# Kernel tuning notes

Hardware: AMD Instinct MI355X
Metric: run time of the kernel (lower is better)

The kernel has to match this reference:

```python
import jax, jax.numpy as jnp
import numpy as np

B, T, D, H = 4, 2048, 1024, 16
DK = DV = 64
R = 64
KS = 4
EPS = 1e-6


def setup_inputs() -> dict:
    key = jax.random.key(0)
    ks = jax.random.split(key, 16)
    def w(k, shape, s=0.02):
        return jax.random.normal(k, shape, jnp.float32) * s
    return {
        "x": jax.random.normal(ks[0], (B, T, D), jnp.float32),
        "conv_q_w": w(ks[1], (D, 1, KS), 0.3), "conv_q_b": jnp.zeros((D,), jnp.float32),
        "conv_k_w": w(ks[2], (D, 1, KS), 0.3), "conv_k_b": jnp.zeros((D,), jnp.float32),
        "conv_v_w": w(ks[3], (D, 1, KS), 0.3), "conv_v_b": jnp.zeros((D,), jnp.float32),
        "Wq": w(ks[4], (D, H * DK)), "bq": jnp.zeros((H * DK,), jnp.float32),
        "Wk": w(ks[5], (D, H * DK)), "bk": jnp.zeros((H * DK,), jnp.float32),
        "Wv": w(ks[6], (D, H * DV)), "bv": jnp.zeros((H * DV,), jnp.float32),
        "W_ad": w(ks[7], (D, R)), "b_ad": jnp.zeros((R,), jnp.float32),
        "W_au": w(ks[8], (R, H * DK)), "b_au": jnp.zeros((H * DK,), jnp.float32),
        "W_beta": w(ks[9], (D, H)), "b_beta": jnp.zeros((H,), jnp.float32),
        "rms_w": jnp.ones((H, DV), jnp.float32),
        "W_gd": w(ks[10], (D, R)), "b_gd": jnp.zeros((R,), jnp.float32),
        "W_gu": w(ks[11], (R, H)), "b_gu": jnp.zeros((H,), jnp.float32),
        "Wo": w(ks[12], (H * DV, D)), "bo": jnp.zeros((D,), jnp.float32),
    }


def _shortconv(x, w, b):
    # causal depthwise conv1d: torch pads (KS-1) both sides then slices [:T] == left-pad KS-1
    xc = jnp.transpose(x, (0, 2, 1))  # [B, D, T]
    y = jax.lax.conv_general_dilated(
        xc, w, (1,), [(KS - 1, 0)],
        dimension_numbers=("NCH", "OIH", "NCH"), feature_group_count=D)
    y = y + b[None, :, None]
    return jax.nn.silu(jnp.transpose(y, (0, 2, 1)))  # [B, T, D]


def _l2(x):
    # x / sqrt(clamp(sum(x^2), eps))  (matches torch clamp_min then sqrt)
    return x / jnp.sqrt(jnp.maximum(jnp.sum(x * x, -1, keepdims=True), EPS))


def _heads(z, dh):
    # [B,T,H*dh] -> [B*H,T,dh]
    return jnp.transpose(z.reshape(B, T, H, dh), (0, 2, 1, 3)).reshape(B * H, T, dh)


def reference(x, conv_q_w, conv_q_b, conv_k_w, conv_k_b, conv_v_w, conv_v_b,
              Wq, bq, Wk, bk, Wv, bv, W_ad, b_ad, W_au, b_au, W_beta, b_beta,
              rms_w, W_gd, b_gd, W_gu, b_gu, Wo, bo):
    qx = _shortconv(x, conv_q_w, conv_q_b)
    kx = _shortconv(x, conv_k_w, conv_k_b)
    vx = _shortconv(x, conv_v_w, conv_v_b)
    Q = _l2(_heads(qx @ Wq + bq, DK))            # [BH,T,DK]
    K = _l2(_heads(kx @ Wk + bk, DK))            # [BH,T,DK]
    V = _heads(vx @ Wv + bv, DV)                 # [BH,T,DV]
    alpha = jax.nn.sigmoid(jax.nn.silu(x @ W_ad + b_ad) @ W_au + b_au)  # [B,T,H*DK]
    A = _heads(alpha, DK)                        # [BH,T,DK]
    beta = jax.nn.sigmoid(x @ W_beta + b_beta)   # [B,T,H]
    Bta = jnp.transpose(beta, (0, 2, 1)).reshape(B * H, T, 1)

    S0 = jnp.zeros((B * H, DK, DV), jnp.float32)

    def step(S, inp):
        q, k, v, a, b = inp                      # [BH,DK],[BH,DK],[BH,DV],[BH,DK],[BH,1]
        S = S * a[:, :, None]                    # gated decay (row scale)
        kTS = jnp.einsum("bi,bij->bj", k, S)    # k^T S : [BH,DV]
        S = S + (b * k)[:, :, None] * (v - kTS)[:, None, :]  # rank-1 delta update
        o = jnp.einsum("bij,bi->bj", S, q)      # S^T q : [BH,DV]
        return S, o

    tm = lambda z: jnp.transpose(z, (1, 0, 2))   # time-major for scan
    S_final, out_t = jax.lax.scan(step, S0, (tm(Q), tm(K), tm(V), tm(A), tm(Bta)))
    O = jnp.transpose(out_t, (1, 0, 2)).reshape(B, H, T, DV)

    # headwise RMSNorm then sigmoid output gate
    var = jnp.mean(O * O, -1, keepdims=True)
    O = O * jax.lax.rsqrt(var + EPS) * rms_w[None, :, None, :]
    gate = jax.nn.sigmoid(jax.nn.silu(x @ W_gd + b_gd) @ W_gu + b_gu)  # [B,T,H]
    O = O * jnp.transpose(gate, (0, 2, 1))[:, :, :, None]

    y = jnp.transpose(O, (0, 2, 1, 3)).reshape(B, T, H * DV) @ Wo + bo
    return y, S_final.reshape(B, H, DK, DV)
```

## Files before the change

### kernel.cpp

```cpp
#include <hip/hip_runtime.h>
#include <hip/hip_bf16.h>
#include <cstdint>

#define BB 4
#define TT 2048
#define DD 1024
#define HH 16
#define NR (BB*TT)
#define CC 16
#define NCH (TT/CC)

typedef __attribute__((ext_vector_type(8))) short bf16x8;
typedef __attribute__((ext_vector_type(4))) float f32x4;
typedef __attribute__((ext_vector_type(4))) unsigned int u32x4;
typedef __attribute__((ext_vector_type(2))) unsigned int u32x2;

#define GLL(g, l, SZ) __builtin_amdgcn_global_load_lds( \
    (const __attribute__((address_space(1))) void*)(uintptr_t)(const void*)(g), \
    (__attribute__((address_space(3))) void*)(uintptr_t)(void*)(l), SZ, 0, 0)

__device__ __forceinline__ unsigned short f2bf(float f) {
  unsigned u = __builtin_bit_cast(unsigned, f);
  unsigned r = 0x7FFFu + ((u >> 16) & 1u);
  return (unsigned short)((u + r) >> 16);
}
__device__ __forceinline__ unsigned pk2(float a, float b) {
  return (unsigned)f2bf(a) | ((unsigned)f2bf(b) << 16);
}
__device__ __forceinline__ float siluf(float v) { return v / (1.f + __expf(-v)); }
__device__ __forceinline__ float sigmf(float v) { return 1.f / (1.f + __expf(-v)); }


__global__ __launch_bounds__(256) void transpose_convert(
    const float* __restrict__ W, unsigned short* __restrict__ Wt, int K, int N) {
  __shared__ float tile[64][65];
  const int tid = threadIdx.x;
  const int bk = blockIdx.x * 64, bn = blockIdx.y * 64;
  const int r = tid >> 2, c4 = (tid & 3) * 16;
#pragma unroll 4
  for (int e = 0; e < 16; ++e)
    tile[r][c4 + e] = W[(size_t)(bk + r) * N + bn + c4 + e];
  __syncthreads();
#pragma unroll 4
  for (int e = 0; e < 16; ++e)
    Wt[(size_t)(bn + r) * K + bk + c4 + e] = f2bf(tile[c4 + e][r]);
}

__global__ void conv_small_T(const float* __restrict__ W, unsigned short* __restrict__ Wt,
                             int K, int N, int Npad) {
  int idx = blockIdx.x * 256 + threadIdx.x;
  if (idx >= Npad * K) return;
  int n = idx / K, k = idx - n * K;
  float v = (n < N) ? W[(size_t)k * N + n] : 0.f;
  Wt[idx] = f2bf(v);
}

__global__ void pack_stage1_T(const float* __restrict__ Wad, const float* __restrict__ Wgd,
                              const float* __restrict__ Wbeta, unsigned short* __restrict__ Wt) {
  int idx = blockIdx.x * 256 + threadIdx.x;
  int n = idx >> 10, k = idx & 1023;
  float v = 0.f;
  if (n < 64) v = Wad[(size_t)k * 64 + n];
  else if (n < 128) v = Wgd[(size_t)k * 64 + (n - 64)];
  else if (n < 144) v = Wbeta[(size_t)k * 16 + (n - 128)];
  Wt[idx] = f2bf(v);
}

__global__ void pack_bias(const float* __restrict__ bad, const float* __restrict__ bgd,
                          const float* __restrict__ bbeta, const float* __restrict__ bgu,
                          float* __restrict__ bst1, float* __restrict__ bgup) {
  int t = threadIdx.x;
  float v = 0.f;
  if (t < 64) v = bad[t];
  else if (t < 128) v = bgd[t - 64];
  else if (t < 144) v = bbeta[t - 128];
  bst1[t] = v;
  if (t < 128) bgup[t] = (t < 16) ? bgu[t] : 0.f;
}

__global__ __launch_bounds__(256) void conv_silu(
    const float* __restrict__ x,
    const float* __restrict__ qw, const float* __restrict__ qb,
    const float* __restrict__ kw, const float* __restrict__ kb,
    const float* __restrict__ vw, const float* __restrict__ vb,
    unsigned short* __restrict__ qx, unsigned short* __restrict__ kx,
    unsigned short* __restrict__ vx, unsigned short* __restrict__ xb) {
  const int n = blockIdx.x;
  const int t = n & (TT - 1);
  const int d0 = threadIdx.x * 4;
  const size_t base = (size_t)n * DD + d0;
  f32x4 zero = {0.f, 0.f, 0.f, 0.f};
  f32x4 x0 = *(const f32x4*)(x + base);
  f32x4 xm1 = (t >= 1) ? *(const f32x4*)(x + base - DD) : zero;
  f32x4 xm2 = (t >= 2) ? *(const f32x4*)(x + base - 2 * DD) : zero;
  f32x4 xm3 = (t >= 3) ? *(const f32x4*)(x + base - 3 * DD) : zero;
  float sq[4], sk[4], sv[4];
#pragma unroll
  for (int e = 0; e < 4; ++e) {
    const int d = d0 + e;
    const f32x4 wq = *(const f32x4*)(qw + (size_t)d * 4);
    const f32x4 wk = *(const f32x4*)(kw + (size_t)d * 4);
    const f32x4 wv = *(const f32x4*)(vw + (size_t)d * 4);
    float aq = wq[0] * xm3[e] + wq[1] * xm2[e] + wq[2] * xm1[e] + wq[3] * x0[e] + qb[d];
    float ak = wk[0] * xm3[e] + wk[1] * xm2[e] + wk[2] * xm1[e] + wk[3] * x0[e] + kb[d];
    float av = wv[0] * xm3[e] + wv[1] * xm2[e] + wv[2] * xm1[e] + wv[3] * x0[e] + vb[d];
    sq[e] = siluf(aq); sk[e] = siluf(ak); sv[e] = siluf(av);
  }
  u32x2 o;
  o[0] = pk2(sq[0], sq[1]); o[1] = pk2(sq[2], sq[3]); *(u32x2*)(qx + base) = o;
  o[0] = pk2(sk[0], sk[1]); o[1] = pk2(sk[2], sk[3]); *(u32x2*)(kx + base) = o;
  o[0] = pk2(sv[0], sv[1]); o[1] = pk2(sv[2], sv[3]); *(u32x2*)(vx + base) = o;
  o[0] = pk2(x0[0], x0[1]); o[1] = pk2(x0[2], x0[3]); *(u32x2*)(xb + base) = o;
}

template <int ACT>
__global__ __launch_bounds__(256) void gemm_bt(
    const unsigned short* __restrict__ A, const unsigned short* __restrict__ Bt,
    const float* __restrict__ bias, float* __restrict__ C,
    int M, int N, int K, int ldc, int nstore) {
  __shared__ unsigned short lsA[128 * 32];
  __shared__ unsigned short lsB[128 * 32];
  const int tid = threadIdx.x;
  const int wid = tid >> 6, lane = tid & 63;
  const int wr = wid >> 1, wc = wid & 1;
  const int m0 = blockIdx.x * 128, n0 = blockIdx.y * 128;
  f32x4 acc[4][4] = {};
  const int nk = K >> 5;
  const int r0 = wid * 32 + (lane >> 2);
  const int cb = (lane & 3) * 16;
  char* lA = (char*)lsA;
  char* lB = (char*)lsB;
  const size_t rowb = (size_t)K * 2;

  for (int kt = 0; kt < nk; ++kt) {
    const char* gA = (const char*)(A + (size_t)(m0 + r0) * K) + kt * 64 + cb;
    const char* gB = (const char*)(Bt + (size_t)(n0 + r0) * K) + kt * 64 + cb;
    GLL(gA, lA + (wid * 32) * 64, 16);
    GLL(gA + 16 * rowb, lA + (wid * 32 + 16) * 64, 16);
    GLL(gB, lB + (wid * 32) * 64, 16);
    GLL(gB + 16 * rowb, lB + (wid * 32 + 16) * 64, 16);
    __syncthreads();
    bf16x8 af[4], bfr[4];
#pragma unroll
    for (int f = 0; f < 4; ++f)
      af[f] = *(const bf16x8*)(lA + (wr * 64 + f * 16 + (lane & 15)) * 64 + (lane >> 4) * 16);
#pragma unroll
    for (int f = 0; f < 4; ++f)
      bfr[f] = *(const bf16x8*)(lB + (wc * 64 + f * 16 + (lane & 15)) * 64 + (lane >> 4) * 16);
#pragma unroll
    for (int i = 0; i < 4; ++i)
#pragma unroll
      for (int j = 0; j < 4; ++j)
        acc[i][j] = __builtin_amdgcn_mfma_f32_16x16x32_bf16(af[i], bfr[j], acc[i][j], 0, 0, 0);
    __syncthreads();
  }
#pragma unroll
  for (int i = 0; i < 4; ++i) {
    const int gr0 = m0 + wr * 64 + i * 16 + (lane >> 4) * 4;
#pragma unroll
    for (int j = 0; j < 4; ++j) {
      const int gc = n0 + wc * 64 + j * 16 + (lane & 15);
      if (gc < nstore) {
        const float bv = bias[gc];
#pragma unroll
        for (int r = 0; r < 4; ++r) {
          float v = acc[i][j][r] + bv;
          if (ACT == 1) v = sigmf(v);
          C[(size_t)(gr0 + r) * ldc + gc] = v;
        }
      }
    }
  }
}

__global__ __launch_bounds__(256) void l2norm_rows(float* __restrict__ Q) {
  const int tid = threadIdx.x;
  const int row = blockIdx.x * 4 + (tid >> 6);
  const int lane = tid & 63;
  float* p = Q + (size_t)row * DD + lane * 16;
  f32x4 v[4];
  float ss = 0.f;
#pragma unroll
  for (int u = 0; u < 4; ++u) {
    v[u] = *(const f32x4*)(p + u * 4);
#pragma unroll
    for (int e = 0; e < 4; ++e) ss = fmaf(v[u][e], v[u][e], ss);
  }
  ss += __shfl_xor(ss, 1);
  ss += __shfl_xor(ss, 2);
  const float rs = 1.f / sqrtf(fmaxf(ss, 1e-6f));
#pragma unroll
  for (int u = 0; u < 4; ++u) {
    f32x4 o;
#pragma unroll
    for (int e = 0; e < 4; ++e) o[e] = v[u][e] * rs;
    *(f32x4*)(p + u * 4) = o;
  }
}

__global__ void prep(const float* __restrict__ s1, unsigned short* __restrict__ ad,
                     unsigned short* __restrict__ gd, float* __restrict__ betaT) {
  const int n = blockIdx.x, t = threadIdx.x;
  float v = s1[(size_t)n * 256 + t];
  if (t < 64) ad[(size_t)n * 64 + t] = f2bf(siluf(v));
  else gd[(size_t)n * 64 + (t - 64)] = f2bf(siluf(v));
  if (t < 16) {
    float b = s1[(size_t)n * 256 + 128 + t];
    int bb = n >> 11, tt = n & (TT - 1);
    betaT[((size_t)(bb * HH + t)) * TT + tt] = sigmf(b);
  }
}

__global__ __launch_bounds__(256) void scan_phaseA(
    float* __restrict__ Qn, float* __restrict__ Kn, float* __restrict__ Vv,
    float* __restrict__ Alp, const float* __restrict__ betaT,
    float* __restrict__ Pbuf, float* __restrict__ bCbuf) {
  __shared__ float bA[CC][68], bKt[CC][68], bKp[CC][68], bQ[CC][68];
  __shared__ float bW1[CC][68], bW2[CC][68], bU1[CC][68], bU2[CC][68];
  __shared__ float Nm[CC][20], Nt[CC][20];
  __shared__ float bet[CC];
  const int bid = (int)blockIdx.x;
  const int bh = bid >> 7, c = bid & 127;
  const int b = bh >> 4, h = bh & 15;
  const int tid = threadIdx.x;
  const int tG = tid >> 4, sA = tid & 15, dG = sA * 4;
  const size_t seg = ((size_t)b * TT) * DD + h * 64;
  const size_t off = seg + (size_t)(c * CC + tG) * DD + dG;

  *(f32x4*)&bA [tG][dG] = *(const f32x4*)(Alp + off);
  *(f32x4*)&bKt[tG][dG] = *(const f32x4*)(Kn  + off);
  *(f32x4*)&bW1[tG][dG] = *(const f32x4*)(Vv  + off);
  *(f32x4*)&bQ [tG][dG] = *(const f32x4*)(Qn  + off);
  if (tid < CC) bet[tid] = betaT[(size_t)bh * TT + c * CC + tid];
  __syncthreads();

  if (tid < 64) {
    float p = bA[0][tid];
#pragma unroll
    for (int t = 1; t < CC; ++t) { p *= bA[t][tid]; bA[t][tid] = p; }
  }
  __syncthreads();

  {
    f32x4 bb = *(f32x4*)&bA[tG][dG];
    f32x4 kk = *(f32x4*)&bKt[tG][dG];
    f32x4 qq = *(f32x4*)&bQ[tG][dG];
    f32x4 vv = *(f32x4*)&bW1[tG][dG];
    f32x4 bC = *(f32x4*)&bA[CC - 1][dG];
    const float bt = bet[tG];
    f32x4 kt, kp, qt, w1, w2, kb;
#pragma unroll
    for (int e = 0; e < 4; ++e) {
      float inv = 1.0f / bb[e];
      kt[e] = kk[e] * bb[e];
      kp[e] = kk[e] * inv;
      qt[e] = qq[e] * bb[e];
      w1[e] = bt * vv[e];
      w2[e] = bt * kt[e];
      kb[e] = kp[e] * bC[e];
    }
    *(f32x4*)&bKt[tG][dG] = kt;
    *(f32x4*)&bKp[tG][dG] = kp;
    *(f32x4*)&bQ [tG][dG] = qt;
    *(f32x4*)&bW1[tG][dG] = w1;
    *(f32x4*)&bW2[tG][dG] = w2;
    *(f32x4*)(Qn + off) = qt;
    *(f32x4*)(Alp + off) = kb;
    if (tid < 64) bCbuf[((size_t)bh * 128 + c) * 64 + tid] = bA[CC - 1][tid];
  }
  __syncthreads();

  {
    f32x4 da = {0.f, 0.f, 0.f, 0.f}, dp = {0.f, 0.f, 0.f, 0.f};
#pragma unroll
    for (int ii = 0; ii < 16; ++ii) {
      f32x4 y = *(f32x4*)&bKp[sA][ii * 4];
      da += (*(f32x4*)&bKt[tG][ii * 4]) * y;
      dp += (*(f32x4*)&bQ [tG][ii * 4]) * y;
    }
    float dotA = (da[0] + da[1]) + (da[2] + da[3]);
    float dotP = (dp[0] + dp[1]) + (dp[2] + dp[3]);
    Nm[tG][sA] = (sA < tG) ? (-bet[tG] * dotA) : 0.f;
    Pbuf[((size_t)bh * 128 + c) * 256 + tG * 16 + sA] = (sA <= tG) ? dotP : 0.f;
  }
  __syncthreads();

#define NEUM2(Pw, I1, I2, O1, O2)                                        \
    {                                                                    \
      f32x4 a1 = *(f32x4*)&I1[tG][dG];                                   \
      f32x4 a2 = *(f32x4*)&I2[tG][dG];                                   \
      for (int s4 = 0; s4 < 4; ++s4) {                                   \
        f32x4 pv = *(f32x4*)&Pw[tG][s4 * 4];                             \
        _Pragma("unroll")                                                \
        for (int e = 0; e < 4; ++e) {                                    \
          a1 += pv[e] * (*(f32x4*)&I1[s4 * 4 + e][dG]);                  \
          a2 += pv[e] * (*(f32x4*)&I2[s4 * 4 + e][dG]);                  \
        }                                                                \
      }                                                                  \
      *(f32x4*)&O1[tG][dG] = a1;                                         \
      *(f32x4*)&O2[tG][dG] = a2;                                         \
    }
#define SQMAT(Pw, Pout)                                                  \
    {                                                                    \
      float acc = 0.f;                                                   \
      _Pragma("unroll")                                                  \
      for (int s = 0; s < 16; ++s) acc = fmaf(Pw[tG][s], Pw[s][sA], acc);\
      Pout[tG][sA] = acc;                                                \
    }

  NEUM2(Nm, bW1, bW2, bU1, bU2)
  SQMAT(Nm, Nt)
  __syncthreads();
  NEUM2(Nt, bU1, bU2, bW1, bW2)
  SQMAT(Nt, Nm)
  __syncthreads();
  NEUM2(Nm, bW1, bW2, bU1, bU2)
  SQMAT(Nm, Nt)
  __syncthreads();
  {
    f32x4 a1 = *(f32x4*)&bU1[tG][dG];
    f32x4 a2 = *(f32x4*)&bU2[tG][dG];
    for (int s4 = 0; s4 < 4; ++s4) {
      f32x4 pv = *(f32x4*)&Nt[tG][s4 * 4];
#pragma unroll
      for (int e = 0; e < 4; ++e) {
        a1 += pv[e] * (*(f32x4*)&bU1[s4 * 4 + e][dG]);
        a2 += pv[e] * (*(f32x4*)&bU2[s4 * 4 + e][dG]);
      }
    }
    *(f32x4*)(Vv + off) = a1;
    *(f32x4*)(Kn + off) = a2;
  }
#undef NEUM2
#undef SQMAT
}

__global__ __launch_bounds__(256, 1) void scan_phaseB(
    const float* __restrict__ W1g, const float* __restrict__ W2g,
    const float* __restrict__ Qt, const float* __restrict__ Kb,
    const float* __restrict__ Pbuf, const float* __restrict__ bCbuf,
    float* __restrict__ O, float* __restrict__ Sout) {
  __shared__ float S0[64][17];
  __shared__ float Um[16][17];
  __shared__ float pw2[2][16][68];
  __shared__ float pqt[2][16][68];
  __shared__ float pkb[2][16][68];
  __shared__ float pP [2][16][20];
  __shared__ float pbC[2][64];
  const int blk = (int)blockIdx.x;
  const int bh = blk >> 2, cg = blk & 3;
  const int b = bh >> 4, h = bh & 15;
  const int tid = threadIdx.x;
  const int T = tid >> 4, j = tid & 15;
  const int jg = cg * 16 + j;
  const size_t seg = ((size_t)b * TT) * DD + h * 64;

  const int lr = T, lq = j;

#define PLOAD(c, W2R, QTR, KBR, PR, BCR)                                    \
  {                                                                         \
    const size_t rb = seg + (size_t)((c) * CC + lr) * DD + lq * 4;          \
    W2R = *(const f32x4*)(W2g + rb);                                        \
    QTR = *(const f32x4*)(Qt + rb);                                         \
    KBR = *(const f32x4*)(Kb + rb);                                         \
    PR  = Pbuf[((size_t)bh * 128 + (c)) * 256 + tid];                       \
    BCR = (tid < 64) ? bCbuf[((size_t)bh * 128 + (c)) * 64 + tid] : 0.f;    \
  }
#define PSTORE(bufI, W2R, QTR, KBR, PR, BCR)                                \
  {                                                                         \
    *(f32x4*)&pw2[bufI][lr][lq * 4] = W2R;                                  \
    *(f32x4*)&pqt[bufI][lr][lq * 4] = QTR;                                  \
    *(f32x4*)&pkb[bufI][lr][lq * 4] = KBR;                                  \
    pP[bufI][T][j] = PR;                                                    \
    if (tid < 64) pbC[bufI][tid] = BCR;                                     \
  }

  {
    f32x4 w2r, qtr, kbr; float pr, bcr;
    PLOAD(0, w2r, qtr, kbr, pr, bcr)
    PSTORE(0, w2r, qtr, kbr, pr, bcr)
  }
#pragma unroll
  for (int r = 0; r < 4; ++r) S0[T * 4 + r][j] = 0.f;
  __syncthreads();

  for (int c = 0; c < NCH; ++c) {
    const int buf = c & 1;
    f32x4 w2n, qtn, kbn; float pn, bcn;
    const bool more = (c + 1 < NCH);
    if (more) PLOAD(c + 1, w2n, qtn, kbn, pn, bcn)
    const float w1v = W1g[seg + (size_t)(c * CC + T) * DD + jg];

    float u0 = 0.f, u1 = 0.f, q0 = 0.f, q1 = 0.f;
#pragma unroll
    for (int k4 = 0; k4 < 16; ++k4) {
      f32x4 wv = *(const f32x4*)&pw2[buf][T][k4 * 4];
      f32x4 qv = *(const f32x4*)&pqt[buf][T][k4 * 4];
      float s0 = S0[k4 * 4 + 0][j], s1 = S0[k4 * 4 + 1][j];
      float s2 = S0[k4 * 4 + 2][j], s3 = S0[k4 * 4 + 3][j];
      u0 = fmaf(-wv[0], s0, u0); q0 = fmaf(qv[0], s0, q0);
      u1 = fmaf(-wv[1], s1, u1); q1 = fmaf(qv[1], s1, q1);
      u0 = fmaf(-wv[2], s2, u0); q0 = fmaf(qv[2], s2, q0);
      u1 = fmaf(-wv[3], s3, u1); q1 = fmaf(qv[3], s3, q1);
    }
    Um[T][j] = w1v + u0 + u1;
    __syncthreads();

    float um[CC];
#pragma unroll
    for (int s = 0; s < CC; ++s) um[s] = Um[s][j];

    float o = q0 + q1;
#pragma unroll
    for (int s4 = 0; s4 < 4; ++s4) {
      f32x4 pv = *(const f32x4*)&pP[buf][T][s4 * 4];
      o = fmaf(pv[0], um[s4 * 4 + 0], o);
      o = fmaf(pv[1], um[s4 * 4 + 1], o);
      o = fmaf(pv[2], um[s4 * 4 + 2], o);
      o = fmaf(pv[3], um[s4 * 4 + 3], o);
    }
    O[seg + (size_t)(c * CC + T) * DD + jg] = o;

    f32x4 bcv = *(const f32x4*)&pbC[buf][T * 4];
    float sp0 = bcv[0] * S0[4 * T + 0][j];
    float sp1 = bcv[1] * S0[4 * T + 1][j];
    float sp2 = bcv[2] * S0[4 * T + 2][j];
    float sp3 = bcv[3] * S0[4 * T + 3][j];
#pragma unroll
    for (int s = 0; s < CC; ++s) {
      f32x4 kv = *(const f32x4*)&pkb[buf][s][T * 4];
      sp0 = fmaf(kv[0], um[s], sp0);
      sp1 = fmaf(kv[1], um[s], sp1);
      sp2 = fmaf(kv[2], um[s], sp2);
      sp3 = fmaf(kv[3], um[s], sp3);
    }
    S0[4 * T + 0][j] = sp0;
    S0[4 * T + 1][j] = sp1;
    S0[4 * T + 2][j] = sp2;
    S0[4 * T + 3][j] = sp3;

    if (more) PSTORE(buf ^ 1, w2n, qtn, kbn, pn, bcn)
    __syncthreads();
  }
#undef PLOAD
#undef PSTORE

#pragma unroll
  for (int r = 0; r < 4; ++r)
    Sout[(size_t)bh * 4096 + (size_t)(4 * T + r) * 64 + jg] = S0[4 * T + r][j];
}

__global__ __launch_bounds__(256) void rms_gate(
    const float* __restrict__ O, const float* __restrict__ rmsw,
    const float* __restrict__ gate, unsigned short* __restrict__ Og) {
  const int tid = threadIdx.x;
  const int row = blockIdx.x * 4 + (tid >> 6);
  const int lane = tid & 63;
  const int h = lane >> 2;
  const float* p = O + (size_t)row * DD + lane * 16;
  f32x4 v[4];
  float ss = 0.f;
#pragma unroll
  for (int u = 0; u < 4; ++u) {
    v[u] = *(const f32x4*)(p + u * 4);
#pragma unroll
    for (int e = 0; e < 4; ++e) ss = fmaf(v[u][e], v[u][e], ss);
  }
  ss += __shfl_xor(ss, 1);
  ss += __shfl_xor(ss, 2);
  const float rs = rsqrtf(ss * (1.f / 64.f) + 1e-6f);
  const float g = gate[row * 16 + h];
  const float* wp = rmsw + h * 64 + (lane & 3) * 16;
  unsigned ow[8];
#pragma unroll
  for (int u = 0; u < 4; ++u) {
    f32x4 wv = *(const f32x4*)(wp + u * 4);
    float a0 = v[u][0] * rs * wv[0] * g, a1 = v[u][1] * rs * wv[1] * g;
    float a2 = v[u][2] * rs * wv[2] * g, a3 = v[u][3] * rs * wv[3] * g;
    ow[u * 2] = pk2(a0, a1);
    ow[u * 2 + 1] = pk2(a2, a3);
  }
  u32x4* dst = (u32x4*)(Og + (size_t)row * DD + lane * 16);
  u32x4 o1, o2;
  o1[0] = ow[0]; o1[1] = ow[1]; o1[2] = ow[2]; o1[3] = ow[3];
  o2[0] = ow[4]; o2[1] = ow[5]; o2[2] = ow[6]; o2[3] = ow[7];
  dst[0] = o1; dst[1] = o2;
}

extern "C" void kernel_launch(void* const* d_in, const int* in_sizes, int n_in,
                              void* d_out, int out_size, void* d_ws, size_t ws_size,
                              hipStream_t stream) {
  const float* x    = (const float*)d_in[0];
  const float* qw   = (const float*)d_in[1];
  const float* qb   = (const float*)d_in[2];
  const float* kw   = (const float*)d_in[3];
  const float* kb   = (const float*)d_in[4];
  const float* vw   = (const float*)d_in[5];
  const float* vb   = (const float*)d_in[6];
  const float* Wq   = (const float*)d_in[7];
  const float* bq   = (const float*)d_in[8];
  const float* Wk   = (const float*)d_in[9];
  const float* bk   = (const float*)d_in[10];
  const float* Wv   = (const float*)d_in[11];
  const float* bv   = (const float*)d_in[12];
  const float* Wad  = (const float*)d_in[13];
  const float* bad  = (const float*)d_in[14];
  const float* Wau  = (const float*)d_in[15];
  const float* bau  = (const float*)d_in[16];
  const float* Wbeta= (const float*)d_in[17];
  const float* bbeta= (const float*)d_in[18];
  const float* rmsw = (const float*)d_in[19];
  const float* Wgd  = (const float*)d_in[20];
  const float* bgd  = (const float*)d_in[21];
  const float* Wgu  = (const float*)d_in[22];
  const float* bgu  = (const float*)d_in[23];
  const float* Wo   = (const float*)d_in[24];
  const float* bo   = (const float*)d_in[25];

  char* ws = (char*)d_ws;
  const size_t MB = 1ull << 20;
  unsigned short* WqT   = (unsigned short*)(ws + 0 * MB);
  unsigned short* WkT   = (unsigned short*)(ws + 2 * MB);
  unsigned short* WvT   = (unsigned short*)(ws + 4 * MB);
  unsigned short* WoT   = (unsigned short*)(ws + 6 * MB);
  unsigned short* WauT  = (unsigned short*)(ws + 8 * MB);
  unsigned short* Wst1T = (unsigned short*)(ws + 8 * MB + 256 * 1024);
  unsigned short* WguT  = (unsigned short*)(ws + 8 * MB + 768 * 1024);
  float* bst1 = (float*)(ws + 8 * MB + 800 * 1024);
  float* bgup = (float*)(ws + 8 * MB + 804 * 1024);
  unsigned short* x_bf = (unsigned short*)(ws + 9 * MB);
  unsigned short* qx   = (unsigned short*)(ws + 25 * MB);
  unsigned short* kx   = (unsigned short*)(ws + 41 * MB);
  unsigned short* vx   = (unsigned short*)(ws + 57 * MB);
  float* Qn    = (float*)(ws + 73 * MB);
  float* Kn    = (float*)(ws + 105 * MB);
  float* Vv    = (float*)(ws + 137 * MB);
  float* stage1= (float*)(ws + 169 * MB);
  unsigned short* adb = (unsigned short*)(ws + 177 * MB);
  unsigned short* gdb = (unsigned short*)(ws + 178 * MB);
  float* betaT = (float*)(ws + 179 * MB);
  float* gate  = (float*)(ws + 179 * MB + 512 * 1024);
  float* bCbuf = (float*)(ws + 180 * MB);
  float* alpha = (float*)(ws + 9 * MB);
  float* Obuf  = (float*)(ws + 41 * MB);
  unsigned short* Og = (unsigned short*)(ws + 137 * MB);
  float* Pbuf  = stage1;
  float* y = (float*)d_out;
  float* Sout = y + (size_t)NR * DD;

  dim3 blk(256);
  transpose_convert<<<dim3(16, 16), blk, 0, stream>>>(Wq, WqT, 1024, 1024);
  transpose_convert<<<dim3(16, 16), blk, 0, stream>>>(Wk, WkT, 1024, 1024);
  transpose_convert<<<dim3(16, 16), blk, 0, stream>>>(Wv, WvT, 1024, 1024);
  transpose_convert<<<dim3(16, 16), blk, 0, stream>>>(Wo, WoT, 1024, 1024);
  conv_small_T<<<dim3(256), blk, 0, stream>>>(Wau, WauT, 64, 1024, 1024);
  pack_stage1_T<<<dim3(1024), blk, 0, stream>>>(Wad, Wgd, Wbeta, Wst1T);
  conv_small_T<<<dim3(32), blk, 0, stream>>>(Wgu, WguT, 64, 16, 128);
  pack_bias<<<dim3(1), blk, 0, stream>>>(bad, bgd, bbeta, bgu, bst1, bgup);

  conv_silu<<<dim3(NR), blk, 0, stream>>>(x, qw, qb, kw, kb, vw, vb, qx, kx, vx, x_bf);

  gemm_bt<0><<<dim3(64, 2), blk, 0, stream>>>(x_bf, Wst1T, bst1, stage1, NR, 256, 1024, 256, 256);
  gemm_bt<0><<<dim3(64, 8), blk, 0, stream>>>(qx, WqT, bq, Qn, NR, 1024, 1024, 1024, 1024);
  gemm_bt<0><<<dim3(64, 8), blk, 0, stream>>>(kx, WkT, bk, Kn, NR, 1024, 1024, 1024, 1024);
  gemm_bt<0><<<dim3(64, 8), blk, 0, stream>>>(vx, WvT, bv, Vv, NR, 1024, 1024, 1024, 1024);
  l2norm_rows<<<dim3(2048), blk, 0, stream>>>(Qn);
  l2norm_rows<<<dim3(2048), blk, 0, stream>>>(Kn);
  prep<<<dim3(NR), dim3(128), 0, stream>>>(stage1, adb, gdb, betaT);
  gemm_bt<1><<<dim3(64, 8), blk, 0, stream>>>(adb, WauT, bau, alpha, NR, 1024, 64, 1024, 1024);
  gemm_bt<1><<<dim3(64, 1), blk, 0, stream>>>(gdb, WguT, bgup, gate, NR, 128, 64, 16, 16);

  scan_phaseA<<<dim3(8192), blk, 0, stream>>>(Qn, Kn, Vv, alpha, betaT, Pbuf, bCbuf);
  scan_phaseB<<<dim3(256), blk, 0, stream>>>(Vv, Kn, Qn, alpha, Pbuf, bCbuf, Obuf, Sout);

  rms_gate<<<dim3(2048), blk, 0, stream>>>(Obuf, rmsw, gate, Og);
  gemm_bt<0><<<dim3(64, 8), blk, 0, stream>>>(Og, WoT, bo, y, NR, 1024, 1024, 1024, 1024);
}
```

Before: 547.8 us.

## Split scan_phaseB across 512 threads with k-dimension halves and split prefetch

The sequential chunk scan kernel now runs 512 threads per block instead of 256. The two halves split the 64-long reduction over S for u and q, with partial sums combined through shared memory, and they also split the S row updates. Prefetch loads are divided between the halves so each thread issues fewer global loads per chunk. This roughly halves per-thread serial work on the latency-bound recurrence, at the cost of extra shared-memory traffic for the partial-sum reduction and with only half the threads computing the output.

```diff
diff --git a/kernel.cpp b/kernel.cpp
--- a/kernel.cpp
+++ b/kernel.cpp
@@ -12,6 +12,7 @@
 
 typedef __attribute__((ext_vector_type(8))) short bf16x8;
 typedef __attribute__((ext_vector_type(4))) float f32x4;
+typedef __attribute__((ext_vector_type(2))) float f32x2;
 typedef __attribute__((ext_vector_type(4))) unsigned int u32x4;
 typedef __attribute__((ext_vector_type(2))) unsigned int u32x2;
 
@@ -335,13 +336,14 @@
 #undef SQMAT
 }
 
-__global__ __launch_bounds__(256, 1) void scan_phaseB(
+__global__ __launch_bounds__(512, 2) void scan_phaseB(
     const float* __restrict__ W1g, const float* __restrict__ W2g,
     const float* __restrict__ Qt, const float* __restrict__ Kb,
     const float* __restrict__ Pbuf, const float* __restrict__ bCbuf,
     float* __restrict__ O, float* __restrict__ Sout) {
   __shared__ float S0[64][17];
-  __shared__ float Um[16][17];
+  __shared__ float pU[2][16][17];
+  __shared__ float pOq[2][16][17];
   __shared__ float pw2[2][16][68];
   __shared__ float pqt[2][16][68];
   __shared__ float pkb[2][16][68];
@@ -349,105 +351,120 @@
   __shared__ float pbC[2][64];
   const int blk = (int)blockIdx.x;
   const int bh = blk >> 2, cg = blk & 3;
-  const int b = bh >> 4, h = bh & 15;
+  const int b = bh >> 4, hh = bh & 15;
   const int tid = threadIdx.x;
-  const int T = tid >> 4, j = tid & 15;
+  const int h = tid >> 8;
+  const int t8 = tid & 255;
+  const int T = t8 >> 4, j = t8 & 15;
   const int jg = cg * 16 + j;
-  const size_t seg = ((size_t)b * TT) * DD + h * 64;
-
-  const int lr = T, lq = j;
-
-#define PLOAD(c, W2R, QTR, KBR, PR, BCR)                                    \
+  const size_t seg = ((size_t)b * TT) * DD + hh * 64;
+
+  const int qr = t8 >> 4, qc = t8 & 15;
+
+#define PLOAD(c, W2R, QTR, KBR, PR, BCR, W1R)                               \
   {                                                                         \
-    const size_t rb = seg + (size_t)((c) * CC + lr) * DD + lq * 4;          \
-    W2R = *(const f32x4*)(W2g + rb);                                        \
-    QTR = *(const f32x4*)(Qt + rb);                                         \
-    KBR = *(const f32x4*)(Kb + rb);                                         \
-    PR  = Pbuf[((size_t)bh * 128 + (c)) * 256 + tid];                       \
-    BCR = (tid < 64) ? bCbuf[((size_t)bh * 128 + (c)) * 64 + tid] : 0.f;    \
+    const size_t rb = seg + (size_t)((c) * CC + qr) * DD + qc * 4;          \
+    if (h == 0) {                                                           \
+      W2R = *(const f32x4*)(W2g + rb);                                      \
+      QTR = *(const f32x4*)(Qt + rb);                                       \
+      W1R = W1g[seg + (size_t)((c) * CC + T) * DD + jg];                    \
+    } else {                                                                \
+      KBR = *(const f32x4*)(Kb + rb);                                       \
+      PR  = Pbuf[((size_t)bh * 128 + (c)) * 256 + t8];                      \
+      BCR = (t8 < 64) ? bCbuf[((size_t)bh * 128 + (c)) * 64 + t8] : 0.f;    \
+    }                                                                       \
   }
 #define PSTORE(bufI, W2R, QTR, KBR, PR, BCR)                                \
   {                                                                         \
-    *(f32x4*)&pw2[bufI][lr][lq * 4] = W2R;                                  \
-    *(f32x4*)&pqt[bufI][lr][lq * 4] = QTR;                                  \
-    *(f32x4*)&pkb[bufI][lr][lq * 4] = KBR;                                  \
-    pP[bufI][T][j] = PR;                                                    \
-    if (tid < 64) pbC[bufI][tid] = BCR;                                     \
-  }
-
+    if (h == 0) {                                                           \
+      *(f32x4*)&pw2[bufI][qr][qc * 4] = W2R;                                \
+      *(f32x4*)&pqt[bufI][qr][qc * 4] = QTR;                                \
+    } else {                                                                \
+      *(f32x4*)&pkb[bufI][qr][qc * 4] = KBR;                                \
+      pP[bufI][qr][qc] = PR;                                                \
+      if (t8 < 64) pbC[bufI][t8] = BCR;                                     \
+    }                                                                       \
+  }
+
+  f32x4 w2r = {}, qtr = {}, kbr = {};
+  float pr = 0.f, bcr = 0.f, w1l = 0.f;
+  PLOAD(0, w2r, qtr, kbr, pr, bcr, w1l)
+  PSTORE(0, w2r, qtr, kbr, pr, bcr)
   {
-    f32x4 w2r, qtr, kbr; float pr, bcr;
-    PLOAD(0, w2r, qtr, kbr, pr, bcr)
-    PSTORE(0, w2r, qtr, kbr, pr, bcr)
-  }
-#pragma unroll
-  for (int r = 0; r < 4; ++r) S0[T * 4 + r][j] = 0.f;
+    int e0 = tid, e1 = tid + 512;
+    S0[e0 >> 4][e0 & 15] = 0.f;
+    S0[e1 >> 4][e1 & 15] = 0.f;
+  }
   __syncthreads();
 
   for (int c = 0; c < NCH; ++c) {
     const int buf = c & 1;
-    f32x4 w2n, qtn, kbn; float pn, bcn;
+    f32x4 w2n = {}, qtn = {}, kbn = {};
+    float pn = 0.f, bcn = 0.f, w1n = 0.f;
     const bool more = (c + 1 < NCH);
-    if (more) PLOAD(c + 1, w2n, qtn, kbn, pn, bcn)
-    const float w1v = W1g[seg + (size_t)(c * CC + T) * DD + jg];
-
-    float u0 = 0.f, u1 = 0.f, q0 = 0.f, q1 = 0.f;
-#pragma unroll
-    for (int k4 = 0; k4 < 16; ++k4) {
-      f32x4 wv = *(const f32x4*)&pw2[buf][T][k4 * 4];
-      f32x4 qv = *(const f32x4*)&pqt[buf][T][k4 * 4];
-      float s0 = S0[k4 * 4 + 0][j], s1 = S0[k4 * 4 + 1][j];
-      float s2 = S0[k4 * 4 + 2][j], s3 = S0[k4 * 4 + 3][j];
+    if (more) PLOAD(c + 1, w2n, qtn, kbn, pn, bcn, w1n)
+
+    float u0 = (h == 0) ? w1l : 0.f, u1 = 0.f, q0 = 0.f, q1 = 0.f;
+#pragma unroll
+    for (int k4 = 0; k4 < 8; ++k4) {
+      const int kk = h * 32 + k4 * 4;
+      f32x4 wv = *(const f32x4*)&pw2[buf][T][kk];
+      f32x4 qv = *(const f32x4*)&pqt[buf][T][kk];
+      float s0 = S0[kk + 0][j], s1 = S0[kk + 1][j];
+      float s2 = S0[kk + 2][j], s3 = S0[kk + 3][j];
       u0 = fmaf(-wv[0], s0, u0); q0 = fmaf(qv[0], s0, q0);
       u1 = fmaf(-wv[1], s1, u1); q1 = fmaf(qv[1], s1, q1);
       u0 = fmaf(-wv[2], s2, u0); q0 = fmaf(qv[2], s2, q0);
       u1 = fmaf(-wv[3], s3, u1); q1 = fmaf(qv[3], s3, q1);
     }
-    Um[T][j] = w1v + u0 + u1;
+    pU[h][T][j] = u0 + u1;
+    pOq[h][T][j] = q0 + q1;
     __syncthreads();
 
     float um[CC];
 #pragma unroll
-    for (int s = 0; s < CC; ++s) um[s] = Um[s][j];
-
-    float o = q0 + q1;
-#pragma unroll
-    for (int s4 = 0; s4 < 4; ++s4) {
-      f32x4 pv = *(const f32x4*)&pP[buf][T][s4 * 4];
-      o = fmaf(pv[0], um[s4 * 4 + 0], o);
-      o = fmaf(pv[1], um[s4 * 4 + 1], o);
-      o = fmaf(pv[2], um[s4 * 4 + 2], o);
-      o = fmaf(pv[3], um[s4 * 4 + 3], o);
-    }
-    O[seg + (size_t)(c * CC + T) * DD + jg] = o;
-
-    f32x4 bcv = *(const f32x4*)&pbC[buf][T * 4];
-    float sp0 = bcv[0] * S0[4 * T + 0][j];
-    float sp1 = bcv[1] * S0[4 * T + 1][j];
-    float sp2 = bcv[2] * S0[4 * T + 2][j];
-    float sp3 = bcv[3] * S0[4 * T + 3][j];
-#pragma unroll
-    for (int s = 0; s < CC; ++s) {
-      f32x4 kv = *(const f32x4*)&pkb[buf][s][T * 4];
-      sp0 = fmaf(kv[0], um[s], sp0);
-      sp1 = fmaf(kv[1], um[s], sp1);
-      sp2 = fmaf(kv[2], um[s], sp2);
-      sp3 = fmaf(kv[3], um[s], sp3);
-    }
-    S0[4 * T + 0][j] = sp0;
-    S0[4 * T + 1][j] = sp1;
-    S0[4 * T + 2][j] = sp2;
-    S0[4 * T + 3][j] = sp3;
+    for (int s = 0; s < CC; ++s) um[s] = pU[0][s][j] + pU[1][s][j];
+
+    if (h == 0) {
+      float o = pOq[0][T][j] + pOq[1][T][j];
+#pragma unroll
+      for (int s4 = 0; s4 < 4; ++s4) {
+        f32x4 pv = *(const f32x4*)&pP[buf][T][s4 * 4];
+        o = fmaf(pv[0], um[s4 * 4 + 0], o);
+        o = fmaf(pv[1], um[s4 * 4 + 1], o);
+        o = fmaf(pv[2], um[s4 * 4 + 2], o);
+        o = fmaf(pv[3], um[s4 * 4 + 3], o);
+      }
+      O[seg + (size_t)(c * CC + T) * DD + jg] = o;
+    }
+
+    {
+      const int r0 = 4 * T + 2 * h;
+      f32x2 bcv = *(const f32x2*)&pbC[buf][r0];
+      float sp0 = bcv[0] * S0[r0 + 0][j];
+      float sp1 = bcv[1] * S0[r0 + 1][j];
+#pragma unroll
+      for (int s = 0; s < CC; ++s) {
+        f32x2 kv = *(const f32x2*)&pkb[buf][s][r0];
+        sp0 = fmaf(kv[0], um[s], sp0);
+        sp1 = fmaf(kv[1], um[s], sp1);
+      }
+      S0[r0 + 0][j] = sp0;
+      S0[r0 + 1][j] = sp1;
+    }
 
     if (more) PSTORE(buf ^ 1, w2n, qtn, kbn, pn, bcn)
     __syncthreads();
+    w1l = w1n;
   }
 #undef PLOAD
 #undef PSTORE
 
-#pragma unroll
-  for (int r = 0; r < 4; ++r)
-    Sout[(size_t)bh * 4096 + (size_t)(4 * T + r) * 64 + jg] = S0[4 * T + r][j];
+  {
+    const int r0 = 4 * T + 2 * h;
+    Sout[(size_t)bh * 4096 + (size_t)(r0 + 0) * 64 + jg] = S0[r0 + 0][j];
+    Sout[(size_t)bh * 4096 + (size_t)(r0 + 1) * 64 + jg] = S0[r0 + 1][j];
+  }
 }
 
 __global__ __launch_bounds__(256) void rms_gate(
@@ -571,7 +588,7 @@
   gemm_bt<1><<<dim3(64, 1), blk, 0, stream>>>(gdb, WguT, bgup, gate, NR, 128, 64, 16, 16);
 
   scan_phaseA<<<dim3(8192), blk, 0, stream>>>(Qn, Kn, Vv, alpha, betaT, Pbuf, bCbuf);
-  scan_phaseB<<<dim3(256), blk, 0, stream>>>(Vv, Kn, Qn, alpha, Pbuf, bCbuf, Obuf, Sout);
+  scan_phaseB<<<dim3(256), dim3(512), 0, stream>>>(Vv, Kn, Qn, alpha, Pbuf, bCbuf, Obuf, Sout);
 
   rms_gate<<<dim3(2048), blk, 0, stream>>>(Obuf, rmsw, gate, Og);
   gemm_bt<0><<<dim3(64, 8), blk, 0, stream>>>(Og, WoT, bo, y, NR, 1024, 1024, 1024, 1024);
```

Result: no change. 542.6 us (-0.9%).
